# Optimization experiments

Hardware: AMD Instinct MI355X
Metric: run time of the kernel (lower is better)

Reference implementation:

```python
import jax, jax.numpy as jnp
import numpy as np

EPS = 1e-5
K_NN = 16

def _lin1d(x, W, b):
    # 1x1 Conv1d: x (B,C,N) -> (B,O,N)
    return jnp.einsum('oc,bcn->bon', W, x) + b[None, :, None]

def _lin2d(x, W, b):
    # 1x1 Conv2d: x (B,C,N,K) -> (B,O,N,K)
    return jnp.einsum('oc,bcnk->bonk', W, x) + b[None, :, None, None]

def _bn2d(x, gamma, beta):
    # train-mode BatchNorm2d over (B, N, K) per channel
    mean = jnp.mean(x, axis=(0, 2, 3), keepdims=True)
    var = jnp.var(x, axis=(0, 2, 3), keepdims=True)
    xh = (x - mean) * jax.lax.rsqrt(var + EPS)
    return gamma[None, :, None, None] * xh + beta[None, :, None, None]

def _knn_idx(pq, ps, k):
    # pq (B,3,N), ps (B,3,M) -> idx (B,N,K) of k nearest support points
    d2 = (jnp.sum(pq * pq, axis=1)[:, :, None]
          + jnp.sum(ps * ps, axis=1)[:, None, :]
          - 2.0 * jnp.einsum('bcn,bcm->bnm', pq, ps))
    _, idx = jax.lax.top_k(-d2, k)
    return idx

def _group(x, idx):
    # x (B,C,M), idx (B,N,K) -> (B,C,N,K)
    return jnp.take_along_axis(x[:, :, None, :], idx[:, None, :, :], axis=3)

def setup_inputs() -> dict:
    key = jax.random.key(0)
    ks = jax.random.split(key, 20)
    B, C, D, N, M, H = 4, 128, 64, 2048, 2048, 256
    s = lambda k, shape, scale: (jax.random.normal(k, shape, dtype=jnp.float32) * scale)
    return {
        'pq': s(ks[0], (B, 3, N), 1.0),
        'fq': s(ks[1], (B, C, N), 1.0),
        'ps': s(ks[2], (B, 3, M), 1.0),
        'fs': s(ks[3], (B, C, M), 1.0),
        'Wq': s(ks[4], (D, C), 0.05), 'bq': jnp.zeros((D,), jnp.float32),
        'Wk': s(ks[5], (D, C), 0.05), 'bk': jnp.zeros((D,), jnp.float32),
        'Wv': s(ks[6], (D, C), 0.05), 'bv': jnp.zeros((D,), jnp.float32),
        'Wp1': s(ks[7], (D, 3), 0.2), 'bp1': jnp.zeros((D,), jnp.float32),
        'gp': jnp.ones((D,), jnp.float32), 'btp': jnp.zeros((D,), jnp.float32),
        'Wp2': s(ks[8], (D, D), 0.05), 'bp2': jnp.zeros((D,), jnp.float32),
        'Wa1': s(ks[9], (H, D), 0.05), 'ba1': jnp.zeros((H,), jnp.float32),
        'ga': jnp.ones((H,), jnp.float32), 'bta': jnp.zeros((H,), jnp.float32),
        'Wa2': s(ks[10], (D, H), 0.05), 'ba2': jnp.zeros((D,), jnp.float32),
        'We': s(ks[11], (C, D), 0.05), 'be': jnp.zeros((C,), jnp.float32),
    }

def reference(pq, fq, ps, fs, Wq, bq, Wk, bk, Wv, bv,
              Wp1, bp1, gp, btp, Wp2, bp2,
              Wa1, ba1, ga, bta, Wa2, ba2, We, be):
    identity = fq
    q = _lin1d(fq, Wq, bq)          # (B,D,N)
    k = _lin1d(fs, Wk, bk)          # (B,D,M)
    v = _lin1d(fs, Wv, bv)          # (B,D,M)
    idx = _knn_idx(pq, ps, K_NN)    # (B,N,K)
    key_g = _group(k, idx)          # (B,D,N,K)
    qk_rel = q[:, :, :, None] - key_g
    pos_rel = pq[:, :, :, None] - _group(ps, idx)  # (B,3,N,K)
    # pos_mlp: conv-bn-relu-conv
    pe = _lin2d(pos_rel, Wp1, bp1)
    pe = jax.nn.relu(_bn2d(pe, gp, btp))
    pe = _lin2d(pe, Wp2, bp2)       # (B,D,N,K)
    # attn_mlp: conv-bn-relu-conv
    a = _lin2d(qk_rel + pe, Wa1, ba1)
    a = jax.nn.relu(_bn2d(a, ga, bta))
    a = _lin2d(a, Wa2, ba2)         # (B,D,N,K)
    attn = jax.nn.softmax(a, axis=-1)
    val = _group(v, idx) + pe       # (B,D,N,K)
    agg = jnp.einsum('bcnk,bcnk->bcn', attn, val)
    return _lin1d(agg, We, be) + identity
```

## Files before the change

kernel.cpp:

```cpp
#include <hip/hip_runtime.h>
#include <stdint.h>

#define NN 2048
#define MM 2048
#define NSAMP 131072

typedef float  fv4 __attribute__((ext_vector_type(4)));
typedef short  bfv8 __attribute__((ext_vector_type(8)));
typedef short  bfv4 __attribute__((ext_vector_type(4)));
typedef unsigned short u16;
typedef unsigned long long u64;

__device__ inline u16 f2bf(float x){
  unsigned u = __float_as_uint(x);
  return (u16)((u + 0x7FFFu + ((u>>16)&1u)) >> 16);
}
__device__ inline float bf2f(u16 u){ return __uint_as_float(((unsigned)u)<<16); }
#define MFMA16 __builtin_amdgcn_mfma_f32_16x16x32_bf16

__global__ __launch_bounds__(256) void k_prep(
    const float* __restrict__ Wq, const float* __restrict__ Wk, const float* __restrict__ Wv,
    const float* __restrict__ Wp2, const float* __restrict__ Wa2, const float* __restrict__ We,
    const float* __restrict__ ps,
    u16* __restrict__ Wqbf, u16* __restrict__ Wkbf, u16* __restrict__ Wvbf,
    u16* __restrict__ Wp2bf, u16* __restrict__ Wa2bf, u16* __restrict__ Webf,
    fv4* __restrict__ psP) {
  int gid = blockIdx.x * 256 + threadIdx.x;
  if (gid < 8192)  { Wqbf[gid] = f2bf(Wq[gid]); Wkbf[gid] = f2bf(Wk[gid]);
                     Wvbf[gid] = f2bf(Wv[gid]); Webf[gid] = f2bf(We[gid]); }
  if (gid < 4096)  Wp2bf[gid] = f2bf(Wp2[gid]);
  if (gid < 16384) Wa2bf[gid] = f2bf(Wa2[gid]);
  if (gid < 8192)  { int b = gid >> 11, m = gid & 2047;
    float x = ps[(b*3+0)*MM + m], y = ps[(b*3+1)*MM + m], z = ps[(b*3+2)*MM + m];
    fv4 p; p.x = x; p.y = y; p.z = z; p.w = x*x + y*y + z*z;
    psP[gid] = p; }
}

__global__ __launch_bounds__(256) void k_qkv(
    const float* __restrict__ fq, const float* __restrict__ fs,
    const u16* __restrict__ Wqbf, const u16* __restrict__ Wkbf, const u16* __restrict__ Wvbf,
    const float* __restrict__ bq, const float* __restrict__ bk, const float* __restrict__ bv,
    float* __restrict__ qT, float* __restrict__ kT, float* __restrict__ vT) {
  __shared__ u16 tile[2][32 * 136];
  int bid = blockIdx.x;
  int b = bid >> 6, p0 = (bid & 63) * 32;
  int t = threadIdx.x;
  int w = t >> 6, l = t & 63, lq = l >> 4, ln = l & 15;
  {
    int cq = t >> 3, n4 = (t & 7) * 4;
    #pragma unroll
    for (int it = 0; it < 4; ++it) {
      int c = it * 32 + cq;
      fv4 vq = *(const fv4*)&fq[(b*128 + c)*2048 + p0 + n4];
      fv4 vs = *(const fv4*)&fs[(b*128 + c)*2048 + p0 + n4];
      #pragma unroll
      for (int j = 0; j < 4; ++j) {
        tile[0][(n4 + j)*136 + c] = f2bf(vq[j]);
        tile[1][(n4 + j)*136 + c] = f2bf(vs[j]);
      }
    }
  }
  bfv8 A[3][4];
  #pragma unroll
  for (int mat = 0; mat < 3; ++mat) {
    const u16* W = mat == 0 ? Wqbf : (mat == 1 ? Wkbf : Wvbf);
    #pragma unroll
    for (int kk = 0; kk < 4; ++kk)
      A[mat][kk] = *(const bfv8*)(W + (w*16 + ln)*128 + kk*32 + lq*8);
  }
  __syncthreads();
  fv4 acc[3][2];
  #pragma unroll
  for (int mat = 0; mat < 3; ++mat) {
    const u16* tl = tile[mat == 0 ? 0 : 1];
    #pragma unroll
    for (int nt = 0; nt < 2; ++nt) {
      fv4 a = {0.f,0.f,0.f,0.f};
      #pragma unroll
      for (int kk = 0; kk < 4; ++kk) {
        bfv8 bb = *(const bfv8*)&tl[(nt*16 + ln)*136 + kk*32 + lq*8];
        a = MFMA16(A[mat][kk], bb, a, 0, 0, 0);
      }
      acc[mat][nt] = a;
    }
  }
  #pragma unroll
  for (int mat = 0; mat < 3; ++mat) {
    float* dst = mat == 0 ? qT : (mat == 1 ? kT : vT);
    const float* bia = mat == 0 ? bq : (mat == 1 ? bk : bv);
    fv4 bq4 = *(const fv4*)&bia[w*16 + lq*4];
    #pragma unroll
    for (int nt = 0; nt < 2; ++nt) {
      fv4 o = acc[mat][nt] + bq4;
      *(fv4*)&dst[(b*NN + p0 + nt*16 + ln)*64 + w*16 + lq*4] = o;
    }
  }
}

__global__ __launch_bounds__(256) void k_knn(
    const float* __restrict__ pq, const fv4* __restrict__ psP,
    int* __restrict__ idxb, float* __restrict__ posPart) {
  __shared__ u64 list[4][512];
  __shared__ u64 win[4][16];
  __shared__ int cnt[4];
  __shared__ float sacc[4][9];

  const int t = threadIdx.x, w = t >> 6, lane = t & 63;
  const int qi = blockIdx.x * 4 + w;
  const int b = qi >> 11, n = qi & 2047;
  const float* pqb = pq + b * 3 * NN;
  const fv4* psb = psP + b * 2048;
  const float qx = pqb[n], qy = pqb[NN + n], qz = pqb[2 * NN + n];
  const float qq = qx * qx + qy * qy + qz * qz;

  unsigned key[32];
  unsigned bkey = 0xFFFFFFFFu; unsigned bj = 0;
  #pragma unroll
  for (int j = 0; j < 32; ++j) {
    fv4 P = psb[lane + 64*j];
    float d2 = qq + P.w - 2.f * (qx * P.x + qy * P.y + qz * P.z);
    unsigned bu = __float_as_uint(d2);
    bu = (bu & 0x80000000u) ? ~bu : (bu | 0x80000000u);
    key[j] = bu;
    if (bu < bkey) { bkey = bu; bj = (unsigned)j; }
  }
  u64 e = (((u64)bkey) << 32) | (unsigned)(lane + 64*(int)bj);

  #pragma unroll
  for (int k = 2; k <= 64; k <<= 1) {
    #pragma unroll
    for (int j = k >> 1; j > 0; j >>= 1) {
      u64 x = __shfl_xor(e, j, 64);
      u64 lo = e < x ? e : x, hi = e < x ? x : e;
      bool up = ((lane & k) == 0);
      bool takeLo = (((lane & j) == 0) == up);
      e = takeLo ? lo : hi;
    }
  }
  const u64 thr = __shfl(e, 15, 64);
  const unsigned T32 = (unsigned)(thr >> 32);

  if (lane == 0) cnt[w] = 0;
  #pragma unroll
  for (int j = 0; j < 32; ++j) {
    if (key[j] <= T32) {
      int p = atomicAdd(&cnt[w], 1);
      if (p < 512) list[w][p] = (((u64)key[j]) << 32) | (unsigned)(lane + 64*j);
    }
  }
  const int C = *(volatile int*)&cnt[w];

  u64 myWin = 0;
  if (C <= 64) {
    u64 v = (lane < C) ? list[w][lane] : ~0ULL;
    #pragma unroll
    for (int k = 2; k <= 64; k <<= 1) {
      #pragma unroll
      for (int j = k >> 1; j > 0; j >>= 1) {
        u64 x = __shfl_xor(v, j, 64);
        u64 lo = v < x ? v : x, hi = v < x ? x : v;
        bool up = ((lane & k) == 0);
        bool takeLo = (((lane & j) == 0) == up);
        v = takeLo ? lo : hi;
      }
    }
    myWin = v;
  } else if (C <= 128) {
    u64 e0 = list[w][lane];
    u64 e1 = (64 + lane < C) ? list[w][64 + lane] : ~0ULL;
    #pragma unroll
    for (unsigned k = 2; k <= 128; k <<= 1) {
      #pragma unroll
      for (unsigned j = k >> 1; j > 0; j >>= 1) {
        if (j < 64) {
          u64 x0 = __shfl_xor(e0, (int)j, 64);
          u64 x1 = __shfl_xor(e1, (int)j, 64);
          bool lower = ((lane & j) == 0);
          bool up0 = (k == 128) ? true : ((lane & k) == 0);
          bool up1 = (k == 128) ? true : ((k == 64) ? false : ((lane & k) == 0));
          e0 = (lower == up0) ? (e0 < x0 ? e0 : x0) : (e0 < x0 ? x0 : e0);
          e1 = (lower == up1) ? (e1 < x1 ? e1 : x1) : (e1 < x1 ? x1 : e1);
        } else {
          u64 lo = e0 < e1 ? e0 : e1, hi = e0 < e1 ? e1 : e0;
          e0 = lo; e1 = hi;
        }
      }
    }
    myWin = e0;
  } else {
    int Cc = C > 512 ? 512 : C;
    for (int i = lane; i < 512; i += 64)
      if (i >= Cc) list[w][i] = ~0ULL;
    for (int r = 0; r < 16; ++r) {
      u64 mv = ~0ULL;
      #pragma unroll
      for (int s5 = 0; s5 < 8; ++s5) {
        u64 x = list[w][s5*64 + lane];
        mv = x < mv ? x : mv;
      }
      #pragma unroll
      for (int off = 1; off <= 32; off <<= 1) {
        u64 x = __shfl_xor(mv, off, 64);
        mv = x < mv ? x : mv;
      }
      #pragma unroll
      for (int s5 = 0; s5 < 8; ++s5)
        if (list[w][s5*64 + lane] == mv) list[w][s5*64 + lane] = ~0ULL;
      if (lane == 0) win[w][r] = mv;
    }
    if (lane < 16) myWin = win[w][lane];
  }

  if (lane < 16) {
    unsigned m = (unsigned)(myWin & 0xFFFFFFFFu);
    idxb[qi * 16 + lane] = (int)m;
    fv4 P = psb[m];
    float r0 = qx - P.x, r1 = qy - P.y, r2 = qz - P.z;
    float s[9];
    s[0] = r0; s[1] = r1; s[2] = r2;
    s[3] = r0*r0; s[4] = r0*r1; s[5] = r0*r2;
    s[6] = r1*r1; s[7] = r1*r2; s[8] = r2*r2;
    #pragma unroll
    for (int off = 1; off <= 8; off <<= 1)
      #pragma unroll
      for (int i = 0; i < 9; ++i) s[i] += __shfl_xor(s[i], off, 64);
    if (lane == 0)
      #pragma unroll
      for (int i = 0; i < 9; ++i) sacc[w][i] = s[i];
  }
  __syncthreads();
  if (t < 9) posPart[blockIdx.x * 12 + t]
      = sacc[0][t] + sacc[1][t] + sacc[2][t] + sacc[3][t];
}

__global__ __launch_bounds__(256) void k_posfinal(
    const float* __restrict__ Wp1, const float* __restrict__ bp1,
    const float* __restrict__ gp, const float* __restrict__ btp,
    const float* __restrict__ posPart, float* __restrict__ Wp1f, float* __restrict__ bp1f) {
  __shared__ float red[4][9];
  __shared__ float st[9];
  int t = threadIdx.x;
  int w = t >> 6, lane = t & 63;
  float s[9];
  #pragma unroll
  for (int i = 0; i < 9; ++i) s[i] = 0.f;
  #pragma unroll
  for (int it = 0; it < 8; ++it) {
    const float* p = posPart + (it * 256 + t) * 12;
    fv4 a = *(const fv4*)p;
    fv4 b4 = *(const fv4*)(p + 4);
    float c8 = p[8];
    s[0]+=a.x; s[1]+=a.y; s[2]+=a.z; s[3]+=a.w;
    s[4]+=b4.x; s[5]+=b4.y; s[6]+=b4.z; s[7]+=b4.w;
    s[8]+=c8;
  }
  #pragma unroll
  for (int off = 32; off > 0; off >>= 1)
    #pragma unroll
    for (int i = 0; i < 9; ++i) s[i] += __shfl_xor(s[i], off, 64);
  if (lane == 0)
    #pragma unroll
    for (int i = 0; i < 9; ++i) red[w][i] = s[i];
  __syncthreads();
  if (t < 9) st[t] = red[0][t] + red[1][t] + red[2][t] + red[3][t];
  __syncthreads();
  if (t < 64) {
    int d = t;
    const float invN = 1.f / (float)NSAMP;
    float m0 = st[0]*invN, m1 = st[1]*invN, m2 = st[2]*invN;
    float C00 = st[3]*invN - m0*m0, C01 = st[4]*invN - m0*m1, C02 = st[5]*invN - m0*m2;
    float C11 = st[6]*invN - m1*m1, C12 = st[7]*invN - m1*m2, C22 = st[8]*invN - m2*m2;
    float w0 = Wp1[d*3], w1 = Wp1[d*3+1], w2 = Wp1[d*3+2];
    float mean = w0*m0 + w1*m1 + w2*m2 + bp1[d];
    float var = w0*w0*C00 + w1*w1*C11 + w2*w2*C22 + 2.f*(w0*w1*C01 + w0*w2*C02 + w1*w2*C12);
    float scale = gp[d] * rsqrtf(var + 1e-5f);
    Wp1f[d*3]   = scale * w0;
    Wp1f[d*3+1] = scale * w1;
    Wp1f[d*3+2] = scale * w2;
    bp1f[d] = btp[d] + scale * (bp1[d] - mean);
  }
}

__global__ __launch_bounds__(256) void k_ystats(
    const float* __restrict__ pq, const float* __restrict__ ps,
    const float* __restrict__ qT, const float* __restrict__ kT, const float* __restrict__ vT,
    const int* __restrict__ idxb,
    const float* __restrict__ Wp1f, const float* __restrict__ bp1f,
    const u16* __restrict__ Wp2bf, const float* __restrict__ bp2,
    u16* __restrict__ yg, u16* __restrict__ valg,
    float* __restrict__ Gpart, float* __restrict__ ySumPart) {
  __shared__ __align__(16) unsigned char smem[21760];
  u16*   hp   = (u16*)smem;
  u16*   y2   = (u16*)(smem + 9216);
  float* r3   = (float*)(smem + 18432);
  float* qc   = (float*)(smem + 19200);
  int*   idxA = (int*)(smem + 20224);
  float* sWp1 = (float*)(smem + 20480);
  float* sbp1 = (float*)(smem + 21248);
  float* sbp2 = (float*)(smem + 21504);

  const int t = threadIdx.x;
  const int w = t >> 6, l = t & 63, lq = l >> 4, ln = l & 15;
  const int d0 = 16*w + lq*4;

  if (t < 192) sWp1[t] = Wp1f[t];
  if (t < 64){ sbp1[t] = bp1f[t]; sbp2[t] = bp2[t]; }

  bfv8 Ape[2];
  #pragma unroll
  for (int kk = 0; kk < 2; ++kk)
    Ape[kk] = *(const bfv8*)(Wp2bf + (16*w + ln)*64 + kk*32 + lq*8);

  fv4 gacc[4];
  #pragma unroll
  for (int nt = 0; nt < 4; ++nt) gacc[nt] = (fv4){0.f,0.f,0.f,0.f};
  float ys[4] = {0.f, 0.f, 0.f, 0.f};
  __syncthreads();

  for (int ch = 0; ch < 2; ++ch) {
    const int p0 = blockIdx.x * 8 + ch * 4;
    const int b  = p0 >> 11;
    const int bN = b * 2048;
    if (t < 64) idxA[t] = idxb[p0*16 + t];
    qc[t] = qT[(p0 + (t>>6))*64 + (t & 63)];
    __syncthreads();
    if (t < 192) { int c = t >> 6, s = t & 63; int n = (p0 + (s>>4)) & 2047;
      r3[c*64 + s] = pq[(b*3+c)*NN + n] - ps[(b*3+c)*MM + idxA[s]]; }
    __syncthreads();
    { int s = t >> 2, iq = t & 3;
      float r0 = r3[s], r1 = r3[64+s], r2 = r3[128+s];
      u16 tmp[16];
      #pragma unroll
      for (int e = 0; e < 16; ++e) { int i = iq*16 + e;
        float v = sbp1[i] + sWp1[i*3]*r0 + sWp1[i*3+1]*r1 + sWp1[i*3+2]*r2;
        tmp[e] = f2bf(fmaxf(v, 0.f)); }
      *(bfv8*)&hp[s*72 + iq*16]     = *(const bfv8*)&tmp[0];
      *(bfv8*)&hp[s*72 + iq*16 + 8] = *(const bfv8*)&tmp[8];
    }
    __syncthreads();
    {
      fv4 pe[4];
      #pragma unroll
      for (int nt = 0; nt < 4; ++nt) {
        fv4 acc = {0.f,0.f,0.f,0.f};
        #pragma unroll
        for (int kk = 0; kk < 2; ++kk) {
          bfv8 bb = *(const bfv8*)&hp[(nt*16 + ln)*72 + kk*32 + lq*8];
          acc = MFMA16(Ape[kk], bb, acc, 0, 0, 0);
        }
        pe[nt] = acc;
      }
      fv4 bp2q = *(const fv4*)&sbp2[d0];
      #pragma unroll
      for (int nt = 0; nt < 4; ++nt) {
        int s = nt*16 + ln;
        int mi = idxA[s];
        fv4 kg = *(const fv4*)(kT + (bN + mi)*64 + d0);
        fv4 vg = *(const fv4*)(vT + (bN + mi)*64 + d0);
        fv4 qv = *(const fv4*)&qc[nt*64 + d0];
        fv4 pv = pe[nt] + bp2q;
        fv4 yv = qv - kg + pv;
        fv4 vv = vg + pv;
        u16 yp[4], vp[4];
        #pragma unroll
        for (int r = 0; r < 4; ++r) {
          yp[r] = f2bf(yv[r]); vp[r] = f2bf(vv[r]);
          y2[(d0 + r)*72 + s] = yp[r];
          ys[r] += yv[r];
        }
        *(bfv4*)&yg[((u64)(p0 + nt)*16 + ln)*64 + d0]   = *(const bfv4*)yp;
        *(bfv4*)&valg[((u64)(p0 + nt)*16 + ln)*64 + d0] = *(const bfv4*)vp;
      }
    }
    __syncthreads();
    #pragma unroll
    for (int kk = 0; kk < 2; ++kk) {
      bfv8 aa = *(const bfv8*)&y2[(16*w + ln)*72 + kk*32 + lq*8];
      #pragma unroll
      for (int nt = 0; nt < 4; ++nt) {
        bfv8 bb = *(const bfv8*)&y2[(nt*16 + ln)*72 + kk*32 + lq*8];
        gacc[nt] = MFMA16(aa, bb, gacc[nt], 0, 0, 0);
      }
    }
    __syncthreads();
  }
  #pragma unroll
  for (int nt = 0; nt < 4; ++nt)
    #pragma unroll
    for (int r = 0; r < 4; ++r)
      Gpart[blockIdx.x*4096 + (16*w + lq*4 + r)*64 + nt*16 + ln] = gacc[nt][r];
  #pragma unroll
  for (int off = 1; off <= 8; off <<= 1) {
    #pragma unroll
    for (int r = 0; r < 4; ++r) ys[r] += __shfl_xor(ys[r], off, 64);
  }
  if (ln == 0) {
    #pragma unroll
    for (int r = 0; r < 4; ++r) ySumPart[blockIdx.x*64 + d0 + r] = ys[r];
  }
}

__global__ __launch_bounds__(256) void k_gred(
    const float* __restrict__ Gpart, const float* __restrict__ ySumPart,
    float* __restrict__ G, float* __restrict__ ySum) {
  __shared__ float red[256];
  int bid = blockIdx.x, t = threadIdx.x;
  int tj = t & 63, st = t >> 6;
  if (bid < 64) {
    int j = bid * 64 + tj;
    float s = 0.f;
    for (int p = st * 256; p < st * 256 + 256; ++p)
      s += Gpart[p*4096 + j];
    red[st * 64 + tj] = s;
    __syncthreads();
    if (t < 64)
      G[bid * 64 + t] = red[t] + red[64 + t] + red[128 + t] + red[192 + t];
  } else {
    float s = 0.f;
    for (int p = st * 256; p < st * 256 + 256; ++p)
      s += ySumPart[p*64 + tj];
    red[st * 64 + tj] = s;
    __syncthreads();
    if (t < 64)
      ySum[t] = red[t] + red[64 + t] + red[128 + t] + red[192 + t];
  }
}

__global__ __launch_bounds__(256) void k_attnfinal(
    const float* __restrict__ Wa1, const float* __restrict__ ba1,
    const float* __restrict__ ga, const float* __restrict__ bta,
    const float* __restrict__ ySum, const float* __restrict__ G,
    u16* __restrict__ Wa1fbf, float* __restrict__ ba1f) {
  __shared__ float red[256];
  __shared__ float mu[64];
  __shared__ float sc[1];
  int h = blockIdx.x, t = threadIdx.x;
  const float invN = 1.f / (float)NSAMP;
  if (t < 64) mu[t] = ySum[t] * invN;
  __syncthreads();
  float acc = 0.f;
  #pragma unroll
  for (int e = 0; e < 16; ++e) {
    int pi = t*16 + e, i = pi >> 6, j = pi & 63;
    float cov = G[pi]*invN - mu[i]*mu[j];
    acc += Wa1[h*64 + i] * Wa1[h*64 + j] * cov;
  }
  red[t] = acc;
  __syncthreads();
  for (int s = 128; s > 0; s >>= 1) { if (t < s) red[t] += red[t + s]; __syncthreads(); }
  float var = red[0];
  __syncthreads();
  red[t] = (t < 64) ? Wa1[h*64 + t] * mu[t] : 0.f;
  __syncthreads();
  for (int s = 128; s > 0; s >>= 1) { if (t < s) red[t] += red[t + s]; __syncthreads(); }
  if (t == 0) {
    float mean  = red[0] + ba1[h];
    float scale = ga[h] * rsqrtf(var + 1e-5f);
    sc[0] = scale;
    ba1f[h] = bta[h] + scale * (ba1[h] - mean);
  }
  __syncthreads();
  if (t < 64) Wa1fbf[h*64 + t] = f2bf(sc[0] * Wa1[h*64 + t]);
}

__global__ __launch_bounds__(256, 4) void k_main(
    const u16* __restrict__ yg, const u16* __restrict__ valg,
    const u16* __restrict__ Wa1fbf, const float* __restrict__ ba1f,
    const u16* __restrict__ Wa2bf, const float* __restrict__ ba2,
    u16* __restrict__ aggbf) {
  __shared__ __align__(16) u16 ha[64 * 264];

  const int t = threadIdx.x;
  const int w = t >> 6, l = t & 63, lq = l >> 4, ln = l & 15;
  const int d0 = 16*w + lq*4;
  const int p0 = blockIdx.x * 4;

  bfv8 yb0[4], yb1[4];
  #pragma unroll
  for (int nt = 0; nt < 4; ++nt) {
    const u16* yp = yg + ((u64)(p0 + nt)*16 + ln)*64;
    yb0[nt] = *(const bfv8*)(yp + lq*8);
    yb1[nt] = *(const bfv8*)(yp + 32 + lq*8);
  }
  bfv4 vv4[4];
  #pragma unroll
  for (int nt = 0; nt < 4; ++nt)
    vv4[nt] = *(const bfv4*)(valg + ((u64)(p0 + nt)*16 + ln)*64 + d0);

  bfv8 A1[4][2], A2[8];
  #pragma unroll
  for (int mt = 0; mt < 4; ++mt)
    #pragma unroll
    for (int kk = 0; kk < 2; ++kk)
      A1[mt][kk] = *(const bfv8*)(Wa1fbf + (64*w + mt*16 + ln)*64 + kk*32 + lq*8);
  #pragma unroll
  for (int kk = 0; kk < 8; ++kk)
    A2[kk] = *(const bfv8*)(Wa2bf + (16*w + ln)*256 + kk*32 + lq*8);
  fv4 bq1[4];
  #pragma unroll
  for (int mt = 0; mt < 4; ++mt)
    bq1[mt] = *(const fv4*)&ba1f[64*w + mt*16 + lq*4];
  const fv4 ba2q = *(const fv4*)&ba2[d0];

  #pragma unroll
  for (int nt = 0; nt < 4; ++nt) {
    int s = nt*16 + ln;
    #pragma unroll
    for (int mt = 0; mt < 4; ++mt) {
      fv4 acc = {0.f,0.f,0.f,0.f};
      acc = MFMA16(A1[mt][0], yb0[nt], acc, 0, 0, 0);
      acc = MFMA16(A1[mt][1], yb1[nt], acc, 0, 0, 0);
      int h0 = 64*w + mt*16 + lq*4;
      fv4 bq = bq1[mt];
      u16 hv[4];
      #pragma unroll
      for (int r = 0; r < 4; ++r) hv[r] = f2bf(fmaxf(acc[r] + bq[r], 0.f));
      *(bfv4*)&ha[s*264 + h0] = *(const bfv4*)hv;
    }
  }
  __syncthreads();
  fv4 acc2[4];
  #pragma unroll
  for (int nt = 0; nt < 4; ++nt) acc2[nt] = (fv4){0.f,0.f,0.f,0.f};
  #pragma unroll
  for (int kk = 0; kk < 8; ++kk) {
    #pragma unroll
    for (int nt = 0; nt < 4; ++nt) {
      bfv8 bb = *(const bfv8*)&ha[(nt*16 + ln)*264 + kk*32 + lq*8];
      acc2[nt] = MFMA16(A2[kk], bb, acc2[nt], 0, 0, 0);
    }
  }
  #pragma unroll
  for (int nt = 0; nt < 4; ++nt) {
    fv4 a = acc2[nt] + ba2q;
    fv4 m = a;
    #pragma unroll
    for (int off = 1; off <= 8; off <<= 1)
      #pragma unroll
      for (int r = 0; r < 4; ++r) m[r] = fmaxf(m[r], __shfl_xor(m[r], off, 16));
    fv4 ee, num;
    #pragma unroll
    for (int r = 0; r < 4; ++r) {
      ee[r] = __expf(a[r] - m[r]);
      num[r] = ee[r] * bf2f((u16)vv4[nt][r]);
    }
    fv4 sum = ee;
    #pragma unroll
    for (int off = 1; off <= 8; off <<= 1)
      #pragma unroll
      for (int r = 0; r < 4; ++r) {
        sum[r] += __shfl_xor(sum[r], off, 16);
        num[r] += __shfl_xor(num[r], off, 16);
      }
    if (ln == 0) {
      u16 o[4];
      #pragma unroll
      for (int r = 0; r < 4; ++r) o[r] = f2bf(num[r] / sum[r]);
      *(bfv4*)&aggbf[(u64)(p0 + nt)*64 + d0] = *(const bfv4*)o;
    }
  }
}

__global__ __launch_bounds__(256) void k_epi(
    const u16* __restrict__ aggbf, const u16* __restrict__ Webf,
    const float* __restrict__ be, const float* __restrict__ fq,
    float* __restrict__ out) {
  const int t = threadIdx.x;
  const int w = t >> 6, l = t & 63, lq = l >> 4, ln = l & 15;
  const int P0 = blockIdx.x * 16;
  const int b  = P0 >> 11;
  const int n0 = P0 & 2047;
  bfv8 EA[2][2];
  #pragma unroll
  for (int mt = 0; mt < 2; ++mt)
    #pragma unroll
    for (int kk = 0; kk < 2; ++kk)
      EA[mt][kk] = *(const bfv8*)(Webf + ((w*2 + mt)*16 + ln)*64 + kk*32 + lq*8);
  const u16* bp = aggbf + (P0 + ln)*64;
  bfv8 b0 = *(const bfv8*)(bp + lq*8);
  bfv8 b1 = *(const bfv8*)(bp + 32 + lq*8);
  fv4 eacc[2];
  #pragma unroll
  for (int mt = 0; mt < 2; ++mt) {
    fv4 a = {0.f,0.f,0.f,0.f};
    a = MFMA16(EA[mt][0], b0, a, 0, 0, 0);
    a = MFMA16(EA[mt][1], b1, a, 0, 0, 0);
    eacc[mt] = a;
  }
  #pragma unroll
  for (int mt = 0; mt < 2; ++mt) {
    int c0 = (w*2 + mt)*16 + lq*4;
    fv4 bev = *(const fv4*)&be[c0];
    #pragma unroll
    for (int r = 0; r < 4; ++r) {
      int c = c0 + r;
      int o = (b*128 + c)*2048 + n0 + ln;
      out[o] = eacc[mt][r] + bev[r] + fq[o];
    }
  }
}

extern "C" void kernel_launch(void* const* d_in, const int* in_sizes, int n_in,
                              void* d_out, int out_size, void* d_ws, size_t ws_size,
                              hipStream_t stream) {
  (void)in_sizes; (void)n_in; (void)out_size; (void)ws_size;
  const float* pq  = (const float*)d_in[0];
  const float* fq  = (const float*)d_in[1];
  const float* ps  = (const float*)d_in[2];
  const float* fs  = (const float*)d_in[3];
  const float* Wq  = (const float*)d_in[4];  const float* bq  = (const float*)d_in[5];
  const float* Wk  = (const float*)d_in[6];  const float* bk  = (const float*)d_in[7];
  const float* Wv  = (const float*)d_in[8];  const float* bv  = (const float*)d_in[9];
  const float* Wp1 = (const float*)d_in[10]; const float* bp1 = (const float*)d_in[11];
  const float* gp  = (const float*)d_in[12]; const float* btp = (const float*)d_in[13];
  const float* Wp2 = (const float*)d_in[14]; const float* bp2 = (const float*)d_in[15];
  const float* Wa1 = (const float*)d_in[16]; const float* ba1 = (const float*)d_in[17];
  const float* ga  = (const float*)d_in[18]; const float* bta = (const float*)d_in[19];
  const float* Wa2 = (const float*)d_in[20]; const float* ba2 = (const float*)d_in[21];
  const float* We  = (const float*)d_in[22]; const float* be  = (const float*)d_in[23];
  float* ws = (float*)d_ws;
  float* qT    = ws;
  float* kT    = ws + 524288;
  float* vT    = ws + 1048576;
  u16*   aggbf = (u16*)(ws + 1572864);
  int*   idxb  = (int*)(ws + 1835008);
  u16*   Wqbf  = (u16*)(ws + 1966080);
  u16*   Wkbf  = (u16*)(ws + 1970176);
  u16*   Wvbf  = (u16*)(ws + 1974272);
  u16*   Webf  = (u16*)(ws + 1978368);
  fv4*   psP   = (fv4*)(ws + 1982464);
  float* Wp1f  = ws + 2015232;
  float* bp1f  = ws + 2015424;
  float* ba1f  = ws + 2015488;
  float* G     = ws + 2015744;
  float* ySum  = ws + 2019840;
  float* ySumP = ws + 2019904;
  u16*   Wp2bf  = (u16*)(ws + 2085440);
  u16*   Wa2bf  = (u16*)(ws + 2087488);
  u16*   Wa1fbf = (u16*)(ws + 2095680);
  float* posPart = ws + 2103872;
  float* Gpart   = ws + 2128448;
  u16*   yg    = (u16*)(ws + 6322752);
  u16*   valg  = (u16*)(ws + 10517056);
  float* out   = (float*)d_out;

  k_prep<<<64, 256, 0, stream>>>(Wq, Wk, Wv, Wp2, Wa2, We, ps,
                                 Wqbf, Wkbf, Wvbf, Wp2bf, Wa2bf, Webf, psP);
  k_qkv<<<256, 256, 0, stream>>>(fq, fs, Wqbf, Wkbf, Wvbf, bq, bk, bv, qT, kT, vT);
  k_knn<<<2048, 256, 0, stream>>>(pq, psP, idxb, posPart);
  k_posfinal<<<1, 256, 0, stream>>>(Wp1, bp1, gp, btp, posPart, Wp1f, bp1f);
  k_ystats<<<1024, 256, 0, stream>>>(pq, ps, qT, kT, vT, idxb, Wp1f, bp1f, Wp2bf, bp2,
                                     yg, valg, Gpart, ySumP);
  k_gred<<<65, 256, 0, stream>>>(Gpart, ySumP, G, ySum);
  k_attnfinal<<<256, 256, 0, stream>>>(Wa1, ba1, ga, bta, ySum, G, Wa1fbf, ba1f);
  k_main<<<2048, 256, 0, stream>>>(yg, valg, Wa1fbf, ba1f, Wa2bf, ba2, aggbf);
  k_epi<<<512, 256, 0, stream>>>(aggbf, Webf, be, fq, out);
}
```

Before: 226.7 us.

## Recompute pos-MLP and y/val in main kernel instead of materializing them

The stats kernel no longer writes the bf16 y and val tensors to global memory. The main attention kernel instead recomputes relative positions, the first pos-MLP layer, the Wp2 MFMA and the gathered k/v terms itself, staging y through LDS. This removes a large global write and reread of intermediates at the cost of duplicated gather and MFMA work and more shared memory per block, which may lower occupancy.

```diff
diff --git a/kernel.cpp b/kernel.cpp
--- a/kernel.cpp
+++ b/kernel.cpp
@@ -283,11 +283,10 @@
 
 __global__ __launch_bounds__(256) void k_ystats(
     const float* __restrict__ pq, const float* __restrict__ ps,
-    const float* __restrict__ qT, const float* __restrict__ kT, const float* __restrict__ vT,
+    const float* __restrict__ qT, const float* __restrict__ kT,
     const int* __restrict__ idxb,
     const float* __restrict__ Wp1f, const float* __restrict__ bp1f,
     const u16* __restrict__ Wp2bf, const float* __restrict__ bp2,
-    u16* __restrict__ yg, u16* __restrict__ valg,
     float* __restrict__ Gpart, float* __restrict__ ySumPart) {
   __shared__ __align__(16) unsigned char smem[21760];
   u16*   hp   = (u16*)smem;
@@ -356,20 +355,10 @@
         int s = nt*16 + ln;
         int mi = idxA[s];
         fv4 kg = *(const fv4*)(kT + (bN + mi)*64 + d0);
-        fv4 vg = *(const fv4*)(vT + (bN + mi)*64 + d0);
         fv4 qv = *(const fv4*)&qc[nt*64 + d0];
-        fv4 pv = pe[nt] + bp2q;
-        fv4 yv = qv - kg + pv;
-        fv4 vv = vg + pv;
-        u16 yp[4], vp[4];
+        fv4 yv = qv - kg + pe[nt] + bp2q;
         #pragma unroll
-        for (int r = 0; r < 4; ++r) {
-          yp[r] = f2bf(yv[r]); vp[r] = f2bf(vv[r]);
-          y2[(d0 + r)*72 + s] = yp[r];
-          ys[r] += yv[r];
-        }
-        *(bfv4*)&yg[((u64)(p0 + nt)*16 + ln)*64 + d0]   = *(const bfv4*)yp;
-        *(bfv4*)&valg[((u64)(p0 + nt)*16 + ln)*64 + d0] = *(const bfv4*)vp;
+        for (int r = 0; r < 4; ++r) { y2[(d0 + r)*72 + s] = f2bf(yv[r]); ys[r] += yv[r]; }
       }
     }
     __syncthreads();
@@ -464,72 +453,140 @@
 }
 
 __global__ __launch_bounds__(256, 4) void k_main(
-    const u16* __restrict__ yg, const u16* __restrict__ valg,
+    const float* __restrict__ pq, const float* __restrict__ ps,
+    const float* __restrict__ qT, const float* __restrict__ kT, const float* __restrict__ vT,
+    const int* __restrict__ idxb,
+    const float* __restrict__ Wp1f, const float* __restrict__ bp1f,
+    const u16* __restrict__ Wp2bf, const float* __restrict__ bp2,
     const u16* __restrict__ Wa1fbf, const float* __restrict__ ba1f,
     const u16* __restrict__ Wa2bf, const float* __restrict__ ba2,
     u16* __restrict__ aggbf) {
-  __shared__ __align__(16) u16 ha[64 * 264];
+  __shared__ __align__(16) unsigned char smem[37120];
+  u16*   hp   = (u16*)smem;
+  u16*   ylds = (u16*)(smem + 9216);
+  u16*   ha   = (u16*)smem;
+  float* r3   = (float*)(smem + 33792);
+  float* qc   = (float*)(smem + 34560);
+  int*   idxA = (int*)(smem + 35584);
+  float* sWp1 = (float*)(smem + 35840);
+  float* sbp1 = (float*)(smem + 36608);
+  float* sbp2 = (float*)(smem + 36864);
 
   const int t = threadIdx.x;
   const int w = t >> 6, l = t & 63, lq = l >> 4, ln = l & 15;
   const int d0 = 16*w + lq*4;
   const int p0 = blockIdx.x * 4;
+  const int b  = p0 >> 11;
+  const int bN = b * 2048;
+
+  if (t < 192) sWp1[t] = Wp1f[t];
+  if (t < 64){ sbp1[t] = bp1f[t]; sbp2[t] = bp2[t]; }
+  if (t < 64) idxA[t] = idxb[p0*16 + t];
+  qc[t] = qT[(p0 + (t>>6))*64 + (t & 63)];
+  __syncthreads();
+
+  if (t < 192) { int c = t >> 6, s = t & 63; int n = (p0 + (s>>4)) & 2047;
+    r3[c*64 + s] = pq[(b*3+c)*NN + n] - ps[(b*3+c)*MM + idxA[s]]; }
+  __syncthreads();
+
+  { int s = t >> 2, iq = t & 3;
+    float r0 = r3[s], r1 = r3[64+s], r2 = r3[128+s];
+    u16 tmp[16];
+    #pragma unroll
+    for (int e = 0; e < 16; ++e) { int i = iq*16 + e;
+      float v = sbp1[i] + sWp1[i*3]*r0 + sWp1[i*3+1]*r1 + sWp1[i*3+2]*r2;
+      tmp[e] = f2bf(fmaxf(v, 0.f)); }
+    *(bfv8*)&hp[s*72 + iq*16]     = *(const bfv8*)&tmp[0];
+    *(bfv8*)&hp[s*72 + iq*16 + 8] = *(const bfv8*)&tmp[8];
+  }
+  __syncthreads();
+
+  u16 vp[4][4];
+  {
+    bfv8 Ape[2];
+    #pragma unroll
+    for (int kk = 0; kk < 2; ++kk)
+      Ape[kk] = *(const bfv8*)(Wp2bf + (16*w + ln)*64 + kk*32 + lq*8);
+    fv4 pe[4];
+    #pragma unroll
+    for (int nt = 0; nt < 4; ++nt) {
+      fv4 acc = {0.f,0.f,0.f,0.f};
+      #pragma unroll
+      for (int kk = 0; kk < 2; ++kk) {
+        bfv8 bb = *(const bfv8*)&hp[(nt*16 + ln)*72 + kk*32 + lq*8];
+        acc = MFMA16(Ape[kk], bb, acc, 0, 0, 0);
+      }
+      pe[nt] = acc;
+    }
+    fv4 bp2q = *(const fv4*)&sbp2[d0];
+    #pragma unroll
+    for (int nt = 0; nt < 4; ++nt) {
+      int s = nt*16 + ln;
+      int mi = idxA[s];
+      fv4 kg = *(const fv4*)(kT + (bN + mi)*64 + d0);
+      fv4 vg = *(const fv4*)(vT + (bN + mi)*64 + d0);
+      fv4 qv = *(const fv4*)&qc[nt*64 + d0];
+      fv4 pv = pe[nt] + bp2q;
+      fv4 yv = qv - kg + pv;
+      fv4 vv = vg + pv;
+      u16 yp[4];
+      #pragma unroll
+      for (int r = 0; r < 4; ++r) { yp[r] = f2bf(yv[r]); vp[nt][r] = f2bf(vv[r]); }
+      *(bfv4*)&ylds[s*72 + d0] = *(const bfv4*)yp;
+    }
+  }
+  __syncthreads();
 
   bfv8 yb0[4], yb1[4];
-  #pragma unroll
-  for (int nt = 0; nt < 4; ++nt) {
-    const u16* yp = yg + ((u64)(p0 + nt)*16 + ln)*64;
-    yb0[nt] = *(const bfv8*)(yp + lq*8);
-    yb1[nt] = *(const bfv8*)(yp + 32 + lq*8);
-  }
-  bfv4 vv4[4];
-  #pragma unroll
-  for (int nt = 0; nt < 4; ++nt)
-    vv4[nt] = *(const bfv4*)(valg + ((u64)(p0 + nt)*16 + ln)*64 + d0);
-
-  bfv8 A1[4][2], A2[8];
-  #pragma unroll
-  for (int mt = 0; mt < 4; ++mt)
-    #pragma unroll
-    for (int kk = 0; kk < 2; ++kk)
-      A1[mt][kk] = *(const bfv8*)(Wa1fbf + (64*w + mt*16 + ln)*64 + kk*32 + lq*8);
-  #pragma unroll
-  for (int kk = 0; kk < 8; ++kk)
-    A2[kk] = *(const bfv8*)(Wa2bf + (16*w + ln)*256 + kk*32 + lq*8);
-  fv4 bq1[4];
-  #pragma unroll
-  for (int mt = 0; mt < 4; ++mt)
-    bq1[mt] = *(const fv4*)&ba1f[64*w + mt*16 + lq*4];
-  const fv4 ba2q = *(const fv4*)&ba2[d0];
-
   #pragma unroll
   for (int nt = 0; nt < 4; ++nt) {
     int s = nt*16 + ln;
-    #pragma unroll
-    for (int mt = 0; mt < 4; ++mt) {
-      fv4 acc = {0.f,0.f,0.f,0.f};
-      acc = MFMA16(A1[mt][0], yb0[nt], acc, 0, 0, 0);
-      acc = MFMA16(A1[mt][1], yb1[nt], acc, 0, 0, 0);
-      int h0 = 64*w + mt*16 + lq*4;
-      fv4 bq = bq1[mt];
-      u16 hv[4];
-      #pragma unroll
-      for (int r = 0; r < 4; ++r) hv[r] = f2bf(fmaxf(acc[r] + bq[r], 0.f));
-      *(bfv4*)&ha[s*264 + h0] = *(const bfv4*)hv;
-    }
-  }
-  __syncthreads();
+    yb0[nt] = *(const bfv8*)&ylds[s*72 + lq*8];
+    yb1[nt] = *(const bfv8*)&ylds[s*72 + 32 + lq*8];
+  }
+  __syncthreads();
+
+  {
+    bfv8 A1[4][2];
+    #pragma unroll
+    for (int mt = 0; mt < 4; ++mt)
+      #pragma unroll
+      for (int kk = 0; kk < 2; ++kk)
+        A1[mt][kk] = *(const bfv8*)(Wa1fbf + (64*w + mt*16 + ln)*64 + kk*32 + lq*8);
+    #pragma unroll
+    for (int nt = 0; nt < 4; ++nt) {
+      int s = nt*16 + ln;
+      #pragma unroll
+      for (int mt = 0; mt < 4; ++mt) {
+        fv4 acc = {0.f,0.f,0.f,0.f};
+        acc = MFMA16(A1[mt][0], yb0[nt], acc, 0, 0, 0);
+        acc = MFMA16(A1[mt][1], yb1[nt], acc, 0, 0, 0);
+        int h0 = 64*w + mt*16 + lq*4;
+        fv4 bq = *(const fv4*)&ba1f[h0];
+        u16 hv[4];
+        #pragma unroll
+        for (int r = 0; r < 4; ++r) hv[r] = f2bf(fmaxf(acc[r] + bq[r], 0.f));
+        *(bfv4*)&ha[s*264 + h0] = *(const bfv4*)hv;
+      }
+    }
+  }
+  __syncthreads();
+
   fv4 acc2[4];
   #pragma unroll
   for (int nt = 0; nt < 4; ++nt) acc2[nt] = (fv4){0.f,0.f,0.f,0.f};
-  #pragma unroll
-  for (int kk = 0; kk < 8; ++kk) {
-    #pragma unroll
-    for (int nt = 0; nt < 4; ++nt) {
-      bfv8 bb = *(const bfv8*)&ha[(nt*16 + ln)*264 + kk*32 + lq*8];
-      acc2[nt] = MFMA16(A2[kk], bb, acc2[nt], 0, 0, 0);
-    }
-  }
+  {
+    #pragma unroll
+    for (int kk = 0; kk < 8; ++kk) {
+      bfv8 A2 = *(const bfv8*)(Wa2bf + (16*w + ln)*256 + kk*32 + lq*8);
+      #pragma unroll
+      for (int nt = 0; nt < 4; ++nt) {
+        bfv8 bb = *(const bfv8*)&ha[(nt*16 + ln)*264 + kk*32 + lq*8];
+        acc2[nt] = MFMA16(A2, bb, acc2[nt], 0, 0, 0);
+      }
+    }
+  }
+  const fv4 ba2q = *(const fv4*)&ba2[d0];
   #pragma unroll
   for (int nt = 0; nt < 4; ++nt) {
     fv4 a = acc2[nt] + ba2q;
@@ -542,7 +599,7 @@
     #pragma unroll
     for (int r = 0; r < 4; ++r) {
       ee[r] = __expf(a[r] - m[r]);
-      num[r] = ee[r] * bf2f((u16)vv4[nt][r]);
+      num[r] = ee[r] * bf2f(vp[nt][r]);
     }
     fv4 sum = ee;
     #pragma unroll
@@ -640,8 +697,6 @@
   u16*   Wa1fbf = (u16*)(ws + 2095680);
   float* posPart = ws + 2103872;
   float* Gpart   = ws + 2128448;
-  u16*   yg    = (u16*)(ws + 6322752);
-  u16*   valg  = (u16*)(ws + 10517056);
   float* out   = (float*)d_out;
 
   k_prep<<<64, 256, 0, stream>>>(Wq, Wk, Wv, Wp2, Wa2, We, ps,
@@ -649,10 +704,11 @@
   k_qkv<<<256, 256, 0, stream>>>(fq, fs, Wqbf, Wkbf, Wvbf, bq, bk, bv, qT, kT, vT);
   k_knn<<<2048, 256, 0, stream>>>(pq, psP, idxb, posPart);
   k_posfinal<<<1, 256, 0, stream>>>(Wp1, bp1, gp, btp, posPart, Wp1f, bp1f);
-  k_ystats<<<1024, 256, 0, stream>>>(pq, ps, qT, kT, vT, idxb, Wp1f, bp1f, Wp2bf, bp2,
-                                     yg, valg, Gpart, ySumP);
+  k_ystats<<<1024, 256, 0, stream>>>(pq, ps, qT, kT, idxb, Wp1f, bp1f, Wp2bf, bp2,
+                                     Gpart, ySumP);
   k_gred<<<65, 256, 0, stream>>>(Gpart, ySumP, G, ySum);
   k_attnfinal<<<256, 256, 0, stream>>>(Wa1, ba1, ga, bta, ySum, G, Wa1fbf, ba1f);
-  k_main<<<2048, 256, 0, stream>>>(yg, valg, Wa1fbf, ba1f, Wa2bf, ba2, aggbf);
+  k_main<<<2048, 256, 0, stream>>>(pq, ps, qT, kT, vT, idxb, Wp1f, bp1f, Wp2bf, bp2,
+                                   Wa1fbf, ba1f, Wa2bf, ba2, aggbf);
   k_epi<<<512, 256, 0, stream>>>(aggbf, Webf, be, fq, out);
 }
```

Result: no change. 229.9 us (+1.4%).
